# Kernel optimization log

Hardware: AMD Instinct MI355X
Metric: run time of the kernel (lower is better)

The kernel has to match this reference:

```python
import jax, jax.numpy as jnp
import numpy as np

B, C, H, W = 8, 21, 512, 512
MAX_M = 0.5   # args.ldam_max_m
S = 30.0      # args.ldam_s


def setup_inputs() -> dict:
    key = jax.random.key(0)
    k1, k2 = jax.random.split(key)
    pred = jax.random.normal(k1, (B, C, H, W), dtype=jnp.float32)
    target = jax.random.randint(k2, (B, H, W), 0, C, dtype=jnp.int32)  # class labels (argmax of one-hot)
    return {"pred": pred, "target": target}


def reference(pred, target):
    labels = target.reshape(-1)  # [N]
    # m_list: per-class pixel counts == sum of one-hot target over (0,2,3)
    counts = jnp.zeros((C,), dtype=pred.dtype).at[labels].add(1.0)
    m_list = 1.0 / jnp.sqrt(jnp.sqrt(counts + 1e-4))
    m_list = m_list * (MAX_M / jnp.max(m_list))

    logits = pred.transpose(0, 2, 3, 1).reshape(-1, C)  # [N, C]
    batch_m = m_list[labels]                            # gather == matmul(m_list, one_hot^T)
    onehot = jax.nn.one_hot(labels, C, dtype=logits.dtype)
    output = logits - batch_m[:, None] * onehot         # subtract margin only at target class

    logp = jax.nn.log_softmax(S * output, axis=-1)
    nll = -jnp.take_along_axis(logp, labels[:, None].astype(jnp.int32), axis=1)[:, 0]
    return jnp.mean(nll)
```

## Files before the change

### kernel.cpp

```cpp
#include <hip/hip_runtime.h>

static constexpr int   Cc  = 21;
static constexpr int   HWn = 512 * 512;
static constexpr int   Nn  = 8 * HWn;
static constexpr float MAXM  = 0.5f;
static constexpr float Sc    = 30.0f;
static constexpr float LOG2E = 1.4426950408889634f;
static constexpr float LN2   = 0.6931471805599453f;

static constexpr int WS_COUNTS = 0;
static constexpr int WS_ACC    = 96;
static constexpr int WS_SM     = 128;

__global__ __launch_bounds__(256) void hist_kernel(const int4* __restrict__ t4,
                                                   int* __restrict__ counts) {
    __shared__ int lh[Cc];
    int t = threadIdx.x;
    if (t < Cc) lh[t] = 0;
    __syncthreads();
    int tid = blockIdx.x * 256 + t;
    int4 v = t4[tid];
    atomicAdd(&lh[v.x], 1);
    atomicAdd(&lh[v.y], 1);
    atomicAdd(&lh[v.z], 1);
    atomicAdd(&lh[v.w], 1);
    __syncthreads();
    if (t < Cc) atomicAdd(&counts[t], lh[t]);
}

__global__ __launch_bounds__(64) void mlist_kernel(const int* __restrict__ counts,
                                                   float* __restrict__ sm2) {
    int t = threadIdx.x;
    float mval = 0.0f;
    if (t < Cc) {
        float cnt = (float)counts[t] + 1e-4f;
        mval = 1.0f / sqrtf(sqrtf(cnt));
    }
    float mx = mval;
    #pragma unroll
    for (int o = 32; o >= 1; o >>= 1) mx = fmaxf(mx, __shfl_down(mx, o));
    mx = __shfl(mx, 0);
    if (t < Cc) sm2[t] = Sc * LOG2E * mval * (MAXM / mx);
}

__global__ __launch_bounds__(256, 2) void loss_kernel(const float* __restrict__ pred,
                                                      const int4* __restrict__ t4,
                                                      const float* __restrict__ smg,
                                                      double* __restrict__ acc) {
    __shared__ float s_sm[Cc];
    __shared__ float wsum[4];
    int t = threadIdx.x;
    if (t < Cc) s_sm[t] = smg[t];
    __syncthreads();

    int tid = blockIdx.x * 256 + t;
    int n0  = tid * 4;
    int b   = n0 >> 18;
    int hw  = n0 & (HWn - 1);
    const float4* p4 = (const float4*)(pred + (size_t)b * Cc * HWn + hw);

    float4 x[Cc];
    #pragma unroll
    for (int c = 0; c < Cc; ++c) x[c] = p4[(size_t)c * (HWn / 4)];

    int4 y4 = t4[tid];
    int ys[4] = {y4.x, y4.y, y4.z, y4.w};
    float smy[4];
    #pragma unroll
    for (int k = 0; k < 4; ++k) smy[k] = s_sm[ys[k]];

    const float S2 = Sc * LOG2E;

    float mx[4] = {-1e30f, -1e30f, -1e30f, -1e30f};
    float vy[4] = {0.f, 0.f, 0.f, 0.f};
    #pragma unroll
    for (int c = 0; c < Cc; ++c) {
        float xs[4] = {x[c].x, x[c].y, x[c].z, x[c].w};
        #pragma unroll
        for (int k = 0; k < 4; ++k) {
            bool  isy = (c == ys[k]);
            float val = fmaf(S2, xs[k], isy ? -smy[k] : 0.0f);
            mx[k] = fmaxf(mx[k], val);
            vy[k] = isy ? val : vy[k];
        }
    }

    float nll2 = 0.0f;
    #pragma unroll
    for (int k = 0; k < 4; ++k) {
        float cb = -mx[k];
        float cy = -smy[k] - mx[k];
        float sum = 0.0f;
        #pragma unroll
        for (int c = 0; c < Cc; ++c) {
            float xs = (k == 0) ? x[c].x : (k == 1) ? x[c].y : (k == 2) ? x[c].z : x[c].w;
            sum += exp2f(fmaf(S2, xs, (c == ys[k]) ? cy : cb));
        }
        nll2 += __log2f(sum) + mx[k] - vy[k];
    }
    float nll = nll2 * LN2;

    #pragma unroll
    for (int o = 32; o >= 1; o >>= 1) nll += __shfl_down(nll, o);

    int wave = t >> 6;
    int lane = t & 63;
    if (lane == 0) wsum[wave] = nll;
    __syncthreads();
    if (t == 0) {
        float bsum = wsum[0] + wsum[1] + wsum[2] + wsum[3];
        atomicAdd(acc, (double)bsum);
    }
}

__global__ void final_kernel(const double* __restrict__ acc, float* __restrict__ out) {
    out[0] = (float)(acc[0] / (double)Nn);
}

extern "C" void kernel_launch(void* const* d_in, const int* in_sizes, int n_in,
                              void* d_out, int out_size, void* d_ws, size_t ws_size,
                              hipStream_t stream) {
    const float* pred   = (const float*)d_in[0];
    const int*   target = (const int*)d_in[1];
    float*       out    = (float*)d_out;

    char* ws = (char*)d_ws;
    int*    counts = (int*)(ws + WS_COUNTS);
    double* acc    = (double*)(ws + WS_ACC);
    float*  sm     = (float*)(ws + WS_SM);

    hipMemsetAsync(d_ws, 0, 256, stream);

    hist_kernel <<<Nn / 4 / 256, 256, 0, stream>>>((const int4*)target, counts);
    mlist_kernel<<<1,            64,  0, stream>>>(counts, sm);
    loss_kernel <<<Nn / 4 / 256, 256, 0, stream>>>(pred, (const int4*)target, sm, acc);
    final_kernel<<<1,            1,   0, stream>>>(acc, out);
}
```

Before: 272.6 us.

## Fuse mlist and final kernels into loss kernel, shrink histogram grid

Folds the per-class margin computation into each loss block, which now recomputes it from the global counts after issuing its prediction loads. The final division moves into the loss kernel via per-block partial sums and a last-block-done counter, which replaces the global double atomic. The histogram kernel uses fewer blocks, each processing eight int4 loads per thread, so fewer global atomics are issued. The aim is to remove two tiny kernel launches and the atomic contention, at the cost of redundant per-block margin math and an extra reduction pass.

```diff
diff --git a/kernel.cpp b/kernel.cpp
--- a/kernel.cpp
+++ b/kernel.cpp
@@ -8,9 +8,12 @@
 static constexpr float LOG2E = 1.4426950408889634f;
 static constexpr float LN2   = 0.6931471805599453f;
 
+static constexpr int HIST_BLOCKS = 256;
+static constexpr int LOSS_BLOCKS = Nn / 4 / 256;
+
 static constexpr int WS_COUNTS = 0;
-static constexpr int WS_ACC    = 96;
-static constexpr int WS_SM     = 128;
+static constexpr int WS_FLAG   = 96;
+static constexpr int WS_PART   = 128;
 
 __global__ __launch_bounds__(256) void hist_kernel(const int4* __restrict__ t4,
                                                    int* __restrict__ counts) {
@@ -18,40 +21,29 @@
     int t = threadIdx.x;
     if (t < Cc) lh[t] = 0;
     __syncthreads();
-    int tid = blockIdx.x * 256 + t;
-    int4 v = t4[tid];
-    atomicAdd(&lh[v.x], 1);
-    atomicAdd(&lh[v.y], 1);
-    atomicAdd(&lh[v.z], 1);
-    atomicAdd(&lh[v.w], 1);
+    int base = blockIdx.x * (256 * 8) + t;
+    #pragma unroll
+    for (int i = 0; i < 8; ++i) {
+        int4 v = t4[base + i * 256];
+        atomicAdd(&lh[v.x], 1);
+        atomicAdd(&lh[v.y], 1);
+        atomicAdd(&lh[v.z], 1);
+        atomicAdd(&lh[v.w], 1);
+    }
     __syncthreads();
     if (t < Cc) atomicAdd(&counts[t], lh[t]);
 }
 
-__global__ __launch_bounds__(64) void mlist_kernel(const int* __restrict__ counts,
-                                                   float* __restrict__ sm2) {
-    int t = threadIdx.x;
-    float mval = 0.0f;
-    if (t < Cc) {
-        float cnt = (float)counts[t] + 1e-4f;
-        mval = 1.0f / sqrtf(sqrtf(cnt));
-    }
-    float mx = mval;
-    #pragma unroll
-    for (int o = 32; o >= 1; o >>= 1) mx = fmaxf(mx, __shfl_down(mx, o));
-    mx = __shfl(mx, 0);
-    if (t < Cc) sm2[t] = Sc * LOG2E * mval * (MAXM / mx);
-}
-
 __global__ __launch_bounds__(256, 2) void loss_kernel(const float* __restrict__ pred,
                                                       const int4* __restrict__ t4,
-                                                      const float* __restrict__ smg,
-                                                      double* __restrict__ acc) {
-    __shared__ float s_sm[Cc];
-    __shared__ float wsum[4];
+                                                      const int* __restrict__ counts,
+                                                      double* __restrict__ partial,
+                                                      unsigned int* __restrict__ flag,
+                                                      float* __restrict__ out) {
+    __shared__ float  s_sm[Cc];
+    __shared__ double wsum[4];
+    __shared__ bool   s_last;
     int t = threadIdx.x;
-    if (t < Cc) s_sm[t] = smg[t];
-    __syncthreads();
 
     int tid = blockIdx.x * 256 + t;
     int n0  = tid * 4;
@@ -64,6 +56,21 @@
     for (int c = 0; c < Cc; ++c) x[c] = p4[(size_t)c * (HWn / 4)];
 
     int4 y4 = t4[tid];
+
+    if (t < 64) {
+        float mval = 0.0f;
+        if (t < Cc) {
+            float cnt = (float)counts[t] + 1e-4f;
+            mval = 1.0f / sqrtf(sqrtf(cnt));
+        }
+        float mx = mval;
+        #pragma unroll
+        for (int o = 32; o >= 1; o >>= 1) mx = fmaxf(mx, __shfl_down(mx, o));
+        mx = __shfl(mx, 0);
+        if (t < Cc) s_sm[t] = Sc * LOG2E * mval * (MAXM / mx);
+    }
+    __syncthreads();
+
     int ys[4] = {y4.x, y4.y, y4.z, y4.w};
     float smy[4];
     #pragma unroll
@@ -105,16 +112,28 @@
 
     int wave = t >> 6;
     int lane = t & 63;
-    if (lane == 0) wsum[wave] = nll;
+    if (lane == 0) wsum[wave] = (double)nll;
     __syncthreads();
     if (t == 0) {
-        float bsum = wsum[0] + wsum[1] + wsum[2] + wsum[3];
-        atomicAdd(acc, (double)bsum);
+        double bsum = wsum[0] + wsum[1] + wsum[2] + wsum[3];
+        partial[blockIdx.x] = bsum;
+        __threadfence();
+        unsigned done = atomicAdd(flag, 1u);
+        s_last = (done == (unsigned)(LOSS_BLOCKS - 1));
     }
-}
+    __syncthreads();
 
-__global__ void final_kernel(const double* __restrict__ acc, float* __restrict__ out) {
-    out[0] = (float)(acc[0] / (double)Nn);
+    if (s_last) {
+        __threadfence();
+        double s = 0.0;
+        for (int i = t; i < LOSS_BLOCKS; i += 256) s += partial[i];
+        #pragma unroll
+        for (int o = 32; o >= 1; o >>= 1) s += __shfl_down(s, o);
+        if ((t & 63) == 0) wsum[t >> 6] = s;
+        __syncthreads();
+        if (t == 0)
+            out[0] = (float)((wsum[0] + wsum[1] + wsum[2] + wsum[3]) / (double)Nn);
+    }
 }
 
 extern "C" void kernel_launch(void* const* d_in, const int* in_sizes, int n_in,
@@ -125,14 +144,13 @@
     float*       out    = (float*)d_out;
 
     char* ws = (char*)d_ws;
-    int*    counts = (int*)(ws + WS_COUNTS);
-    double* acc    = (double*)(ws + WS_ACC);
-    float*  sm     = (float*)(ws + WS_SM);
+    int*          counts  = (int*)(ws + WS_COUNTS);
+    unsigned int* flag    = (unsigned int*)(ws + WS_FLAG);
+    double*       partial = (double*)(ws + WS_PART);
 
-    hipMemsetAsync(d_ws, 0, 256, stream);
+    hipMemsetAsync(d_ws, 0, 128, stream);
 
-    hist_kernel <<<Nn / 4 / 256, 256, 0, stream>>>((const int4*)target, counts);
-    mlist_kernel<<<1,            64,  0, stream>>>(counts, sm);
-    loss_kernel <<<Nn / 4 / 256, 256, 0, stream>>>(pred, (const int4*)target, sm, acc);
-    final_kernel<<<1,            1,   0, stream>>>(acc, out);
+    hist_kernel <<<HIST_BLOCKS, 256, 0, stream>>>((const int4*)target, counts);
+    loss_kernel <<<LOSS_BLOCKS, 256, 0, stream>>>(pred, (const int4*)target,
+                                                  counts, partial, flag, out);
 }
```

Result: slower. 368.3 us (+35.1%).
